# Performance work log

Measured on AMD Instinct MI355X. Metric: run time of the kernel, lower is better.

The kernel has to match this reference:

```python
import jax, jax.numpy as jnp
import numpy as np

N, D = 131072, 512
G, NG = 512, 256  # G groups of equal size NG, contiguous; N == G*NG
MARGIN, LAMBDA_CD, LAMBDA_CDD, LAMBDA_PCC, K_MARGIN = 2.0, 0.0, 1.0, 1.0, 0.02
EPS = 1e-6


def setup_inputs() -> dict:
    key = jax.random.key(0)
    k1, k2, k3, k4 = jax.random.split(key, 4)
    z_r = jax.random.normal(k1, (N, D), jnp.float32)
    z_r = z_r / jnp.linalg.norm(z_r, axis=-1, keepdims=True)
    z_v = jax.random.normal(k2, (N, D), jnp.float32)
    z_v = z_v / jnp.linalg.norm(z_v, axis=-1, keepdims=True)
    labels = jax.random.randint(k3, (N,), 0, 2)
    groups = jnp.repeat(jnp.arange(G), NG)  # contiguous equal-size groups
    var_lens = jax.random.randint(k4, (N,), 0, 10000)
    return {"z_r": z_r, "z_v": z_v, "labels": labels, "groups": groups, "var_lens": var_lens}


def reference(z_r, z_v, labels, groups, var_lens):
    # cosine distance per pair: [N]
    d = 1.0 - jnp.sum(z_r * z_v, axis=-1)

    mb = (labels == 0).astype(d.dtype)
    mp = (labels == 1).astype(d.dtype)
    nb, npos = mb.sum(), mp.sum()
    db_mean = jnp.sum(d * mb) / jnp.maximum(nb, 1.0)
    dp_mean = jnp.sum(d * mp) / jnp.maximum(npos, 1.0)

    l_cd = jnp.where(nb > 0, db_mean, 0.0)
    l_cdd = jnp.where((nb > 0) & (npos > 0),
                      jax.nn.relu(MARGIN + db_mean - dp_mean), 0.0)

    # --- per-group losses, vectorized over G equal-size contiguous groups ---
    d_g = d.reshape(G, NG)                                   # [G, n_g]
    v_g = var_lens.reshape(G, NG).astype(d.dtype)            # [G, n_g]

    # Pearson-style z-score matching loss (torch std is unbiased, ddof=1)
    v_std = jnp.std(v_g, axis=1, ddof=1)
    d_std = jnp.std(d_g, axis=1, ddof=1)
    v_z = (v_g - v_g.mean(axis=1, keepdims=True)) / (v_std + EPS)[:, None]
    d_z = (d_g - d_g.mean(axis=1, keepdims=True)) / (d_std + EPS)[:, None]
    corr_loss = jnp.mean((v_z - d_z) ** 2, axis=1)
    corr_loss = jnp.where((v_std > 0) & (d_std > 0), corr_loss, 0.0)

    # sort each group by var_len
    order = jnp.argsort(v_g, axis=1)
    v_s = jnp.take_along_axis(v_g, order, axis=1)            # [G, n_g]
    d_s = jnp.take_along_axis(d_g, order, axis=1)            # [G, n_g]

    # neighbor monotonicity violation
    neigh_viol = jnp.mean(jax.nn.relu(d_s[:, :-1] - d_s[:, 1:] + K_MARGIN), axis=1)

    # pairwise rank loss: dv[g,i,j] = v_s[g,j] - v_s[g,i] (matches torch unsqueeze(0)-unsqueeze(1))
    dv = v_s[:, None, :] - v_s[:, :, None]                   # [G, n_g, n_g]
    dd = d_s[:, None, :] - d_s[:, :, None]                   # [G, n_g, n_g]
    mask = (dv > 0).astype(d.dtype)
    cnt = mask.sum(axis=(1, 2))
    pair_sum = jnp.sum(jax.nn.relu(K_MARGIN - dd) * mask, axis=(1, 2))
    rank_loss = jnp.where(cnt > 0, pair_sum / jnp.maximum(cnt, 1.0), 0.0)

    group_loss = corr_loss + neigh_viol + rank_loss          # [G]
    # size-weighted sum; all groups have equal size NG -> plain mean
    l_pcc = jnp.mean(group_loss)

    total = LAMBDA_CD * l_cd + LAMBDA_CDD * l_cdd + LAMBDA_PCC * l_pcc
    return total, l_cdd, l_pcc, d
```

## Files before the change

### kernel.cpp

```cpp
#include <hip/hip_runtime.h>

#define NTOT   131072
#define DIMV   512
#define GCNT   512
#define NGRP   256
#define KMARG  0.02f
#define CMARG  2.0f
#define EPSC   1e-6f

typedef float f4 __attribute__((ext_vector_type(4)));

template <int NW, int M>
__device__ __forceinline__ void block_sum_m(float* v, float* red) {
  const int t = threadIdx.x;
#pragma unroll
  for (int m = 0; m < M; ++m) {
#pragma unroll
    for (int off = 32; off; off >>= 1) v[m] += __shfl_down(v[m], off, 64);
  }
  __syncthreads();
  if ((t & 63) == 0) {
#pragma unroll
    for (int m = 0; m < M; ++m) red[(t >> 6) * M + m] = v[m];
  }
  __syncthreads();
#pragma unroll
  for (int m = 0; m < M; ++m) {
    float s = 0.0f;
#pragma unroll
    for (int i = 0; i < NW; ++i) s += red[i * M + m];
    v[m] = s;
  }
}

__device__ __forceinline__ float wave_sum(float v) {
#pragma unroll
  for (int off = 32; off; off >>= 1) v += __shfl_down(v, off, 64);
  return v;
}

__global__ __launch_bounds__(256) void fused_kernel(const float* __restrict__ zr,
                                                    const float* __restrict__ zv,
                                                    const int* __restrict__ labels,
                                                    const int* __restrict__ varl,
                                                    float* __restrict__ dvec,
                                                    float* __restrict__ gout) {
  __shared__ float  red[4 * 4];
  __shared__ float  sd[NGRP];
  __shared__ float2 skv[NGRP];
  __shared__ float  sdat[NGRP];
  const int g = blockIdx.x, t = threadIdx.x;
  const int wave = t >> 6, lane = t & 63;

  const size_t rowbase = (size_t)g * NGRP;
#pragma unroll 2
  for (int it = 0; it < NGRP / 8; ++it) {
    const int rg = it * 8 + wave * 2;
    const size_t row0 = rowbase + rg;
    const f4* r = (const f4*)zr + (row0 << 7);
    const f4* v = (const f4*)zv + (row0 << 7);
    f4 a0 = __builtin_nontemporal_load(r + lane);
    f4 b0 = __builtin_nontemporal_load(v + lane);
    f4 a1 = __builtin_nontemporal_load(r + lane + 64);
    f4 b1 = __builtin_nontemporal_load(v + lane + 64);
    f4 a2 = __builtin_nontemporal_load(r + lane + 128);
    f4 b2 = __builtin_nontemporal_load(v + lane + 128);
    f4 a3 = __builtin_nontemporal_load(r + lane + 192);
    f4 b3 = __builtin_nontemporal_load(v + lane + 192);
    f4 p = a0 * b0 + a1 * b1;
    f4 q = a2 * b2 + a3 * b3;
    float s0 = wave_sum(p.x + p.y + p.z + p.w);
    float s1 = wave_sum(q.x + q.y + q.z + q.w);
    if (lane == 0) {
      const float d0 = 1.0f - s0, d1 = 1.0f - s1;
      sd[rg]     = d0;
      sd[rg + 1] = d1;
      dvec[row0]     = d0;
      dvec[row0 + 1] = d1;
    }
  }
  __syncthreads();

  const int idx = g * NGRP + t;
  const float dv  = sd[t];
  const float vv  = (float)varl[idx];
  const int   lab = labels[idx];

  skv[t] = make_float2(vv, dv);

  float sA[4] = {dv, vv, (lab == 0) ? dv : 0.0f, (lab == 0) ? 1.0f : 0.0f};
  block_sum_m<4, 4>(sA, red);
  const float sumd = sA[0], sumv = sA[1], sb = sA[2], cb = sA[3];
  const float md = sumd * (1.0f / NGRP), mv = sumv * (1.0f / NGRP);

  const float vdev = vv - mv, ddev = dv - md;
  float sB[3] = {vdev * vdev, ddev * ddev, vdev * ddev};
  block_sum_m<4, 3>(sB, red);
  const float svv = sB[0], sdd = sB[1], svd = sB[2];
  const float vstd = sqrtf(svv * (1.0f / (NGRP - 1)));
  const float dstd = sqrtf(sdd * (1.0f / (NGRP - 1)));
  const float iv = 1.0f / (vstd + EPSC), id = 1.0f / (dstd + EPSC);
  float corr = (svv * iv * iv + sdd * id * id - 2.0f * svd * iv * id) * (1.0f / NGRP);
  corr = (vstd > 0.0f && dstd > 0.0f) ? corr : 0.0f;

  int rank = 0;
  float pc = 0.0f, ps = 0.0f;
  const float pre = KMARG + dv;
  for (int j = 0; j < NGRP; ++j) {
    const float2 kv = skv[j];
    const float vj = kv.x, dj = kv.y;
    if (vj > vv) {
      pc += 1.0f;
      ps += fmaxf(pre - dj, 0.0f);
    }
    rank += (vj < vv || (vj == vv && j < t)) ? 1 : 0;
  }
  sdat[rank] = dv;
  __syncthreads();
  const float nv = (t < NGRP - 1) ? fmaxf(sdat[t] - sdat[t + 1] + KMARG, 0.0f) : 0.0f;

  float sC[3] = {ps, pc, nv};
  block_sum_m<4, 3>(sC, red);
  const float rank_loss = (sC[1] > 0.0f) ? sC[0] / fmaxf(sC[1], 1.0f) : 0.0f;
  const float neigh = sC[2] * (1.0f / (NGRP - 1));

  if (t == 0) {
    gout[g]            = corr + neigh + rank_loss;
    gout[GCNT + g]     = sb;
    gout[2 * GCNT + g] = cb;
    gout[3 * GCNT + g] = sumd;
  }
}

__global__ __launch_bounds__(512) void final_kernel(const float* __restrict__ gout,
                                                    float* __restrict__ out) {
  __shared__ float red[8 * 4];
  const int t = threadIdx.x;
  float s[4] = {gout[t], gout[GCNT + t], gout[2 * GCNT + t], gout[3 * GCNT + t]};
  block_sum_m<8, 4>(s, red);
  if (t == 0) {
    const float L = s[0], SB = s[1], CB = s[2], SumD = s[3];
    const float SP = SumD - SB;
    const float CP = (float)NTOT - CB;
    const float db = SB / fmaxf(CB, 1.0f);
    const float dp = SP / fmaxf(CP, 1.0f);
    const float l_cdd = (CB > 0.0f && CP > 0.0f) ? fmaxf(CMARG + db - dp, 0.0f) : 0.0f;
    const float l_pcc = L * (1.0f / GCNT);
    out[0] = l_cdd + l_pcc;
    out[1] = l_cdd;
    out[2] = l_pcc;
  }
}

extern "C" void kernel_launch(void* const* d_in, const int* in_sizes, int n_in,
                              void* d_out, int out_size, void* d_ws, size_t ws_size,
                              hipStream_t stream) {
  const float* zr     = (const float*)d_in[0];
  const float* zv     = (const float*)d_in[1];
  const int*   labels = (const int*)d_in[2];
  const int*   varl   = (const int*)d_in[4];
  float* out  = (float*)d_out;
  float* dvec = out + 3;
  float* gws  = (float*)d_ws;

  fused_kernel<<<GCNT, 256, 0, stream>>>(zr, zv, labels, varl, dvec, gws);
  final_kernel<<<1, 512, 0, stream>>>(gws, out);
}
```

Before: 113.8 us.

## Split each row across 16-lane subgroups with DPP row reductions and deeper loads

The dot-product phase now gives each row to a 16-lane DPP row instead of a whole wave. Each lane loads eight float4 pairs per iteration, so four rows are in flight per wave. The 64-lane shuffle reduction is replaced by four DPP row_shr adds, and launch bounds request two blocks per CU. Loads are no longer nontemporal, and the d output uses a nontemporal store. The aim is more memory-level parallelism and less reduction overhead in a bandwidth-bound phase, at the cost of more registers per thread.

```diff
diff --git a/kernel.cpp b/kernel.cpp
--- a/kernel.cpp
+++ b/kernel.cpp
@@ -1,7 +1,6 @@
 #include <hip/hip_runtime.h>
 
 #define NTOT   131072
-#define DIMV   512
 #define GCNT   512
 #define NGRP   256
 #define KMARG  0.02f
@@ -9,6 +8,19 @@
 #define EPSC   1e-6f
 
 typedef float f4 __attribute__((ext_vector_type(4)));
+
+template <int CTRL>
+__device__ __forceinline__ float dpp_add(float v) {
+  const int t = __builtin_amdgcn_update_dpp(0, __float_as_int(v), CTRL, 0xF, 0xF, true);
+  return v + __int_as_float(t);
+}
+__device__ __forceinline__ float row16_sum(float v) {
+  v = dpp_add<0x111>(v);
+  v = dpp_add<0x112>(v);
+  v = dpp_add<0x114>(v);
+  v = dpp_add<0x118>(v);
+  return v;
+}
 
 template <int NW, int M>
 __device__ __forceinline__ void block_sum_m(float* v, float* red) {
@@ -33,50 +45,47 @@
   }
 }
 
-__device__ __forceinline__ float wave_sum(float v) {
-#pragma unroll
-  for (int off = 32; off; off >>= 1) v += __shfl_down(v, off, 64);
-  return v;
-}
-
-__global__ __launch_bounds__(256) void fused_kernel(const float* __restrict__ zr,
-                                                    const float* __restrict__ zv,
-                                                    const int* __restrict__ labels,
-                                                    const int* __restrict__ varl,
-                                                    float* __restrict__ dvec,
-                                                    float* __restrict__ gout) {
+__global__ __launch_bounds__(256, 2) void fused_kernel(const float* __restrict__ zr,
+                                                       const float* __restrict__ zv,
+                                                       const int* __restrict__ labels,
+                                                       const int* __restrict__ varl,
+                                                       float* __restrict__ dvec,
+                                                       float* __restrict__ gout) {
   __shared__ float  red[4 * 4];
   __shared__ float  sd[NGRP];
   __shared__ float2 skv[NGRP];
   __shared__ float  sdat[NGRP];
   const int g = blockIdx.x, t = threadIdx.x;
   const int wave = t >> 6, lane = t & 63;
+  const int l16 = lane & 15, sub = lane >> 4;
+  const size_t rowbase = (size_t)g * NGRP;
 
-  const size_t rowbase = (size_t)g * NGRP;
-#pragma unroll 2
-  for (int it = 0; it < NGRP / 8; ++it) {
-    const int rg = it * 8 + wave * 2;
-    const size_t row0 = rowbase + rg;
-    const f4* r = (const f4*)zr + (row0 << 7);
-    const f4* v = (const f4*)zv + (row0 << 7);
-    f4 a0 = __builtin_nontemporal_load(r + lane);
-    f4 b0 = __builtin_nontemporal_load(v + lane);
-    f4 a1 = __builtin_nontemporal_load(r + lane + 64);
-    f4 b1 = __builtin_nontemporal_load(v + lane + 64);
-    f4 a2 = __builtin_nontemporal_load(r + lane + 128);
-    f4 b2 = __builtin_nontemporal_load(v + lane + 128);
-    f4 a3 = __builtin_nontemporal_load(r + lane + 192);
-    f4 b3 = __builtin_nontemporal_load(v + lane + 192);
-    f4 p = a0 * b0 + a1 * b1;
-    f4 q = a2 * b2 + a3 * b3;
-    float s0 = wave_sum(p.x + p.y + p.z + p.w);
-    float s1 = wave_sum(q.x + q.y + q.z + q.w);
-    if (lane == 0) {
-      const float d0 = 1.0f - s0, d1 = 1.0f - s1;
-      sd[rg]     = d0;
-      sd[rg + 1] = d1;
-      dvec[row0]     = d0;
-      dvec[row0 + 1] = d1;
+#pragma unroll 1
+  for (int it = 0; it < 16; ++it) {
+    const int rg = it * 16 + wave * 4 + sub;
+    const f4* ra = (const f4*)zr + ((rowbase + (size_t)rg) << 7);
+    const f4* rb = (const f4*)zv + ((rowbase + (size_t)rg) << 7);
+    f4 A[8], B[8];
+#pragma unroll
+    for (int k = 0; k < 8; ++k) A[k] = ra[l16 + 16 * k];
+#pragma unroll
+    for (int k = 0; k < 8; ++k) {
+      const int kk = (k + 4) & 7;
+      B[kk] = rb[l16 + 16 * kk];
+    }
+    f4 e = A[0] * B[0] + A[2] * B[2];
+    f4 o = A[1] * B[1] + A[3] * B[3];
+    e += A[4] * B[4];
+    o += A[5] * B[5];
+    e += A[6] * B[6];
+    o += A[7] * B[7];
+    const f4 s4 = e + o;
+    float s = (s4.x + s4.y) + (s4.z + s4.w);
+    s = row16_sum(s);
+    if (l16 == 15) {
+      const float dval = 1.0f - s;
+      sd[rg] = dval;
+      __builtin_nontemporal_store(dval, dvec + rowbase + rg);
     }
   }
   __syncthreads();
```

Measured after the change: 130.8 us. 1.15x slower.
